# Optimization experiments

Hardware: AMD Instinct MI355X
Metric: run time of the kernel (lower is better)

## Reference

```python
import jax, jax.numpy as jnp
import numpy as np

B, N, IN, HID, RANK, POOL = 128, 512, 512, 512, 64, 8


def setup_inputs() -> dict:
    key = jax.random.key(0)
    ks = jax.random.split(key, 7)
    tree_embedding = jax.random.normal(ks[0], (B, N, IN), dtype=jnp.float32)
    # valid top-down tree: parent(i) < i, parent(0) arbitrary (unused: buffers are zero at t=0)
    rng = np.random.default_rng(0)
    node_connection = jnp.asarray(
        rng.integers(0, np.maximum(np.arange(N), 1), size=(B, N)), dtype=jnp.int32)
    node_mask = jnp.ones((B, N), dtype=bool)
    s = 0.05
    # gate axis g: 0=f, 1=o, 2=z (three DecomposedBilinear modules stacked)
    wl = jax.random.normal(ks[1], (3, POOL, RANK, IN), dtype=jnp.float32) * s
    wr = jax.random.normal(ks[2], (3, POOL, RANK, HID), dtype=jnp.float32) * s
    wo = jax.random.normal(ks[3], (3, HID, POOL), dtype=jnp.float32) * s
    ul = jax.random.normal(ks[4], (3, HID, IN), dtype=jnp.float32) * s   # use_linear on left input
    ur = jax.random.normal(ks[5], (3, HID, HID), dtype=jnp.float32) * s  # use_linear on parent h
    bias = jax.random.normal(ks[6], (3, HID), dtype=jnp.float32) * s    # use_bias
    return dict(tree_embedding=tree_embedding, node_connection=node_connection,
                node_mask=node_mask, wl=wl, wr=wr, wo=wo, ul=ul, ur=ur, bias=bias)


def _gates(emb, ph, wl, wr, wo, ul, ur, bias):
    # Decomposed bilinear for all 3 gates at once.
    # emb: (B, IN), ph: (B, HID)
    lw = jnp.einsum('bi,gpri->gbpr', emb, wl)
    rw = jnp.einsum('bh,gprh->gbpr', ph, wr)
    pooled = jnp.sum(lw * rw, axis=-1)                       # (g, B, POOL)
    out = jnp.einsum('gbp,ghp->gbh', pooled, wo)             # bilinear term
    out = out + jnp.einsum('bi,ghi->gbh', emb, ul)           # linear(left)
    out = out + jnp.einsum('bh,gkh->gbk', ph, ur)            # linear(right); zero when ph==0 (root)
    out = out + bias[:, None, :]
    return out


def _forward(tree_embedding, node_connection, wl, wr, wo, ul, ur, bias):
    batch, node_num, _ = tree_embedding.shape
    hid = wo.shape[1]
    h0 = jnp.zeros((batch, node_num, hid), tree_embedding.dtype)
    c0 = jnp.zeros_like(h0)
    emb_seq = jnp.swapaxes(tree_embedding, 0, 1)   # (N, B, IN)
    par_seq = jnp.swapaxes(node_connection, 0, 1)  # (N, B)

    def step(carry, xs):
        h_buf, c_buf = carry
        t, emb, par = xs
        idx = par[:, None, None].astype(jnp.int32)
        ph = jnp.take_along_axis(h_buf, idx, axis=1)[:, 0]  # parent gather; zeros at t==0
        pc = jnp.take_along_axis(c_buf, idx, axis=1)[:, 0]
        g = _gates(emb, ph, wl, wr, wo, ul, ur, bias)
        f = jax.nn.sigmoid(g[0])
        o = jax.nn.sigmoid(g[1])
        z = jnp.tanh(g[2])
        c = pc * f + (1.0 - f) * z
        h = o * jnp.tanh(c)
        return (h_buf.at[:, t].set(h), c_buf.at[:, t].set(c)), None

    (h_buf, _), _ = jax.lax.scan(step, (h0, c0),
                                 (jnp.arange(node_num), emb_seq, par_seq))
    return h_buf


def reference(tree_embedding, node_connection, node_mask, wl, wr, wo, ul, ur, bias):
    # node_mask is only threaded through the returned state in the torch code; unused here.
    return _forward(tree_embedding, node_connection, wl, wr, wo, ul, ur, bias)
```

## Files before the change

kernel.cpp:

```cpp
#include <hip/hip_runtime.h>

#define NB 128
#define NN 512
#define NODES (NB * NN)
#define NLEVELS 32

typedef __attribute__((ext_vector_type(8))) short short8;
typedef __attribute__((ext_vector_type(4))) short short4v;
typedef __attribute__((ext_vector_type(4))) float f32x4;
typedef unsigned int u32;

__device__ __forceinline__ float bf2f(short s) {
    union { u32 u; float f; } v;
    v.u = ((u32)(unsigned short)s) << 16;
    return v.f;
}
__device__ __forceinline__ short f2bf(float f) {
    union { u32 u; float f; } v;
    v.f = f;
    u32 u = v.u + 0x7FFFu + ((v.u >> 16) & 1u);
    return (short)(u >> 16);
}
__device__ __forceinline__ float fclamp(float x, float lo, float hi) {
    return fminf(fmaxf(x, lo), hi);
}
__device__ __forceinline__ float fsig(float x) {
    return __builtin_amdgcn_rcpf(1.f + __builtin_amdgcn_exp2f(-1.44269504f * x));
}
__device__ __forceinline__ float ftanh(float x) {
    return 1.f - 2.f * __builtin_amdgcn_rcpf(1.f + __builtin_amdgcn_exp2f(2.88539008f * x));
}
#define MFMA16(a, b, c) __builtin_amdgcn_mfma_f32_16x16x32_bf16((a), (b), (c), 0, 0, 0)

__device__ __forceinline__ void gl16(const void* g, void* l) {
    __builtin_amdgcn_global_load_lds(
        (const __attribute__((address_space(1))) unsigned int*)g,
        (__attribute__((address_space(3))) unsigned int*)l,
        16, 0, 0);
}

#define WAIT_VMCNT(n) asm volatile("s_waitcnt vmcnt(" #n ")" ::: "memory")
#define PIPE_BAR()                                  \
    do {                                            \
        __builtin_amdgcn_sched_barrier(0);          \
        __builtin_amdgcn_s_barrier();               \
        __builtin_amdgcn_sched_barrier(0);          \
    } while (0)

__global__ __launch_bounds__(256) void conv_emb_kernel(
    const float* __restrict__ src, const u32* __restrict__ pos_g,
    short* __restrict__ dst)
{
    int i = blockIdx.x * 256 + threadIdx.x;
    const int stride = gridDim.x * 256;
    for (; i < NODES * 64; i += stride) {
        const int node = i >> 6;
        const int o = (i & 63) << 3;
        const u32 dr = pos_g[node];
        const float* s = src + ((size_t)node << 9) + o;
        short8 v;
#pragma unroll
        for (int j = 0; j < 8; j++) v[j] = f2bf(s[j]);
        *(short8*)((char*)dst + ((size_t)dr << 10) + ((size_t)o << 1)) = v;
    }
}

__global__ __launch_bounds__(256) void wpack_lin_kernel(
    const float* __restrict__ ul, const float* __restrict__ ur,
    short* __restrict__ img)
{
    int gid = blockIdx.x * 256 + threadIdx.x;
    const int stride = gridDim.x * 256;
    for (; gid < 196608; gid += stride) {
        const int cgkc = gid / 1536;
        const int d = (gid - cgkc * 1536) << 4;
        const int cg = cgkc >> 4, kc = cgkc & 15;
        const int u = d ^ (((d >> 7) & 7) << 4);
        const int p = u >> 7;
        const int koff = u & 127;
        const int row = ((p >> 6) << 9) + (cg << 6) + (p & 63);
        const float* src = (kc < 8 ? ul : ur) + (size_t)row * 512
                         + ((kc & 7) << 6) + (koff >> 1);
        short8 o;
#pragma unroll
        for (int i = 0; i < 8; i++) o[i] = f2bf(src[i]);
        *(short8*)((char*)img + (size_t)cgkc * 24576 + d) = o;
    }
}
__global__ __launch_bounds__(256) void wpack_pool_kernel(
    const float* __restrict__ wl, const float* __restrict__ wr,
    short* __restrict__ imgL, short* __restrict__ imgR)
{
    int gid = blockIdx.x * 256 + threadIdx.x;
    const int stride = gridDim.x * 256;
    for (; gid < 196608; gid += stride) {
        const int tensor = gid >= 98304;
        const int g2 = gid - tensor * 98304;
        const int sc = g2 / 512;
        const int d = (g2 - sc * 512) << 4;
        const int s = sc >> 3, ch = sc & 7;
        const int slot = d >> 10;
        const int l = (d >> 4) & 63;
        const int col = (slot << 3) + (l >> 3);
        const int eoff = ((l & 7) ^ (col & 7)) << 3;
        const float* src = (tensor ? wr : wl)
                         + (size_t)(s * 64 + col) * 512 + (ch << 6) + eoff;
        short8 o;
#pragma unroll
        for (int i = 0; i < 8; i++) o[i] = f2bf(src[i]);
        short* dst = tensor ? imgR : imgL;
        *(short8*)((char*)dst + (size_t)sc * 8192 + d) = o;
    }
}

__global__ __launch_bounds__(256) void zero_kernel(int* __restrict__ counts)
{
    const int i = blockIdx.x * 256 + threadIdx.x;
    if (i < 520) counts[i] = 0;
}

__global__ __launch_bounds__(256) void depth_kernel(
    const int* __restrict__ conn,
    unsigned char* __restrict__ lvl_g,
    int* __restrict__ counts)
{
    __shared__ short anc[NN];
    __shared__ short dep[NN];
    __shared__ int hist[520];
    const int b = blockIdx.x;
    const int tid = threadIdx.x;

    for (int i = tid; i < 520; i += 256) hist[i] = 0;
    for (int i = tid; i < NN; i += 256) {
        anc[i] = (i == 0) ? (short)0 : (short)conn[b * NN + i];
        dep[i] = (i == 0) ? (short)0 : (short)1;
    }
    __syncthreads();
    for (int it = 0; it < 9; it++) {
        const int i0 = tid, i1 = tid + 256;
        const short a0 = anc[i0], d0 = dep[i0];
        const short a1 = anc[i1], d1 = dep[i1];
        const short da0 = dep[a0], aa0 = anc[a0];
        const short da1 = dep[a1], aa1 = anc[a1];
        __syncthreads();
        dep[i0] = (short)(d0 + da0); anc[i0] = aa0;
        dep[i1] = (short)(d1 + da1); anc[i1] = aa1;
        __syncthreads();
    }
    for (int i = tid; i < NN; i += 256) {
        const unsigned char d = (unsigned char)dep[i];
        lvl_g[b * NN + i] = d;
        atomicAdd(&hist[d], 1);
    }
    __syncthreads();
    for (int i = tid; i < 520; i += 256)
        if (hist[i]) atomicAdd(&counts[i], hist[i]);
}

__global__ __launch_bounds__(256) void scan_kernel(
    const int* __restrict__ counts,
    int* __restrict__ offs,
    int* __restrict__ cursor)
{
    __shared__ int c[520];
    __shared__ int o[520];
    const int tid = threadIdx.x;
    for (int i = tid; i < 520; i += 256) c[i] = counts[i];
    __syncthreads();
    if (tid == 0) {
        int acc = 0;
        for (int l = 0; l < 520; l++) { o[l] = acc; acc += c[l]; }
    }
    __syncthreads();
    for (int i = tid; i < 520; i += 256) {
        offs[i] = o[i];
        cursor[i] = o[i];
    }
}

__global__ __launch_bounds__(256) void scatter_kernel(
    const int* __restrict__ conn,
    const unsigned char* __restrict__ lvl_g,
    int* __restrict__ cursor,
    u32* __restrict__ list,
    u32* __restrict__ pos_g,
    u32* __restrict__ plist)
{
    __shared__ int hist[520];
    __shared__ int base_s[520];
    __shared__ short rank_s[NN];
    __shared__ int pos_s[NN];
    const int b = blockIdx.x;
    const int tid = threadIdx.x;

    for (int i = tid; i < 520; i += 256) hist[i] = 0;
    __syncthreads();
    for (int i = tid; i < NN; i += 256) {
        const int l = lvl_g[b * NN + i];
        rank_s[i] = (short)atomicAdd(&hist[l], 1);
    }
    __syncthreads();
    for (int i = tid; i < 520; i += 256) {
        const int c = hist[i];
        base_s[i] = c ? atomicAdd(&cursor[i], c) : 0;
    }
    __syncthreads();
    for (int i = tid; i < NN; i += 256) {
        const int l = lvl_g[b * NN + i];
        pos_s[i] = base_s[l] + rank_s[i];
    }
    __syncthreads();
    for (int i = tid; i < NN; i += 256) {
        const int par = (i == 0) ? 0 : conn[b * NN + i];
        const int pos = pos_s[i];
        list[pos] = ((u32)b << 18) | ((u32)i << 9) | (u32)par;
        plist[pos] = (u32)pos_s[par];
        pos_g[b * NN + i] = (u32)pos;
    }
}

__global__ __launch_bounds__(256, 2) void pool_kernel(
    const int lvl,
    const short* __restrict__ emb_lvl,
    const short* __restrict__ imgL,
    const short* __restrict__ imgR,
    const short* __restrict__ h_lvl,
    const int* __restrict__ offs,
    const u32* __restrict__ plist,
    float* __restrict__ pooled2)
{
    const int base = offs[lvl];
    const int M = offs[lvl + 1] - base;
    if (M <= 0) return;
    const int nt = (M + 63) >> 6;

    const int s = blockIdx.x % 24;
    const int rb = blockIdx.x / 24;
    const int nb = gridDim.x / 24;
    if (rb >= nt) return;

    __shared__ __attribute__((aligned(16))) char lds[2][32768];

    const int tid = threadIdx.x;
    const int l = tid & 63;
    const int w = tid >> 6;
    const int q = l >> 4;
    const int ln = l & 15;

    const char* bL = (const char*)imgL + (size_t)s * 65536 + (l << 4);
    const char* bR = (const char*)imgR + (size_t)s * 65536 + (l << 4);

    for (int tm = rb; tm < nt; tm += nb) {
        const int m0 = tm << 6;
        const char* pAe[2];
        const char* pAh[2];
#pragma unroll
        for (int cc = 0; cc < 2; cc++) {
            const int row = ((2 * w + cc) << 3) + (l >> 3);
            const int koff = ((l & 7) ^ (row & 7)) << 4;
            int mr = m0 + row; if (mr > M - 1) mr = M - 1;
            pAe[cc] = (const char*)emb_lvl + ((size_t)(base + mr) << 10) + koff;
            pAh[cc] = (const char*)h_lvl + ((size_t)plist[base + mr] << 10) + koff;
        }

        f32x4 accL[4], accR[4];
#pragma unroll
        for (int jj = 0; jj < 4; jj++) {
            accL[jj] = {0.f, 0.f, 0.f, 0.f};
            accR[jj] = {0.f, 0.f, 0.f, 0.f};
        }

        {
            char* L = lds[0];
#pragma unroll
            for (int cc = 0; cc < 2; cc++) {
                const int slt = (2 * w + cc) << 10;
                gl16(pAe[cc], L + slt);
                gl16(pAh[cc], L + 8192 + slt);
                gl16(bL + slt, L + 16384 + slt);
                gl16(bR + slt, L + 24576 + slt);
            }
        }

        for (int c = 0; c < 8; c++) {
            if (c < 7) {
                char* L = lds[(c + 1) & 1];
                const int cb = (c + 1) << 7;
                const size_t ib = (size_t)(c + 1) << 13;
#pragma unroll
                for (int cc = 0; cc < 2; cc++) {
                    const int slt = (2 * w + cc) << 10;
                    gl16(pAe[cc] + cb, L + slt);
                    gl16(pAh[cc] + cb, L + 8192 + slt);
                    gl16(bL + ib + slt, L + 16384 + slt);
                    gl16(bR + ib + slt, L + 24576 + slt);
                }
                WAIT_VMCNT(8);
            } else {
                WAIT_VMCNT(0);
            }
            PIPE_BAR();
            const char* L = lds[c & 1];
#pragma unroll
            for (int kf = 0; kf < 2; kf++) {
                const int abyte = (((w << 4) + ln) << 7) + (kf << 6) + (q << 4);
                const int aswz = abyte ^ ((ln & 7) << 4);
                const short8 ae = *(const short8*)(L + aswz);
                const short8 ah = *(const short8*)(L + 8192 + aswz);
#pragma unroll
                for (int jj = 0; jj < 4; jj++) {
                    const int bbyte = (((jj << 4) + ln) << 7) + (kf << 6) + (q << 4);
                    const int bswz = bbyte ^ ((ln & 7) << 4);
                    const short8 bl = *(const short8*)(L + 16384 + bswz);
                    const short8 br = *(const short8*)(L + 24576 + bswz);
                    accL[jj] = MFMA16(ae, bl, accL[jj]);
                    accR[jj] = MFMA16(ah, br, accR[jj]);
                }
            }
            PIPE_BAR();
        }

#pragma unroll
        for (int reg = 0; reg < 4; reg++) {
            float v = accL[0][reg] * accR[0][reg] + accL[1][reg] * accR[1][reg]
                    + accL[2][reg] * accR[2][reg] + accL[3][reg] * accR[3][reg];
            v += __shfl_xor(v, 1, 64);
            v += __shfl_xor(v, 2, 64);
            v += __shfl_xor(v, 4, 64);
            v += __shfl_xor(v, 8, 64);
            if (ln == 0) {
                const int mr = m0 + (w << 4) + (q << 2) + reg;
                if (mr < M) pooled2[(size_t)mr * 24 + s] = v;
            }
        }
    }
}

__global__ __launch_bounds__(256, 2) void gemm_lin_kernel(
    const int lvl,
    const short* __restrict__ emb_lvl,
    const short* __restrict__ Blin,
    const float* __restrict__ wo,
    const float* __restrict__ bias,
    const int* __restrict__ offs,
    const u32* __restrict__ list,
    const u32* __restrict__ plist,
    const float* __restrict__ pooled2,
    float* __restrict__ h_out,
    short* __restrict__ h_lvl,
    short* __restrict__ c_lvl)
{
    const int base = offs[lvl];
    const int M = offs[lvl + 1] - base;
    if (M <= 0) return;
    const int nt = (M + 127) >> 7;
    const int nkc = (lvl > 0) ? 16 : 8;

    __shared__ __attribute__((aligned(16))) char lds[2][24576];

    const int tid = threadIdx.x;
    const int lane = tid & 63;
    const int w = tid >> 6;
    const int q = lane >> 4;
    const int ln = lane & 15;
    const int x = blockIdx.x & 7;
    const int jb = blockIdx.x >> 3;
    const int cg = jb & 7;
    const int tslot = jb >> 3;
    const int swzc = (ln & 7) << 4;

    const char* pB = (const char*)Blin + (size_t)cg * 393216 + (lane << 4);

    const int wrow0 = w << 5;

    for (int tm = x + (tslot << 3); tm < nt; tm += 96) {
        const int m0 = tm << 7;
        const char *pE0, *pE1, *pH0, *pH1;
        {
            int r0 = m0 + wrow0 + ln;      if (r0 > M - 1) r0 = M - 1;
            int r1 = m0 + wrow0 + 16 + ln; if (r1 > M - 1) r1 = M - 1;
            const int qo = q << 4;
            pE0 = (const char*)emb_lvl + ((size_t)(base + r0) << 10) + qo;
            pE1 = (const char*)emb_lvl + ((size_t)(base + r1) << 10) + qo;
            pH0 = (const char*)h_lvl + ((size_t)plist[base + r0] << 10) + qo;
            pH1 = (const char*)h_lvl + ((size_t)plist[base + r1] << 10) + qo;
        }

        f32x4 acc[2][12];
#pragma unroll
        for (int ms = 0; ms < 2; ms++)
#pragma unroll
            for (int j = 0; j < 12; j++)
                acc[ms][j] = {0.f, 0.f, 0.f, 0.f};

        {
            char* LB = lds[0];
#pragma unroll
            for (int c = 0; c < 6; c++)
                gl16(pB + ((w * 6 + c) << 10), LB + ((w * 6 + c) << 10));
        }
        short8 c00 = *(const short8*)(pE0);
        short8 c01 = *(const short8*)(pE0 + 64);
        short8 c10 = *(const short8*)(pE1);
        short8 c11 = *(const short8*)(pE1 + 64);
        __syncthreads();

        for (int kc = 0; kc < nkc; kc++) {
            const int kn = (kc + 1 < nkc) ? kc + 1 : kc;
            const char* r0 = (kn < 8) ? pE0 : pH0;
            const char* r1 = (kn < 8) ? pE1 : pH1;
            const int cbn = (kn & 7) << 7;
            short8 n00 = *(const short8*)(r0 + cbn);
            short8 n01 = *(const short8*)(r0 + cbn + 64);
            short8 n10 = *(const short8*)(r1 + cbn);
            short8 n11 = *(const short8*)(r1 + cbn + 64);
            if (kc + 1 < nkc) {
                const size_t ib = (size_t)(kc + 1) * 24576;
                char* LB = lds[(kc + 1) & 1];
#pragma unroll
                for (int c = 0; c < 6; c++)
                    gl16(pB + ib + ((w * 6 + c) << 10), LB + ((w * 6 + c) << 10));
            }
            const char* LB = lds[kc & 1];
#pragma unroll
            for (int ks = 0; ks < 2; ks++) {
                const short8 af0 = ks ? c01 : c00;
                const short8 af1 = ks ? c11 : c10;
                const int kb = (ks << 6) + (q << 4);
#pragma unroll
                for (int j = 0; j < 12; j++) {
                    const short8 bf = *(const short8*)(LB + ((((j * 16 + ln) << 7) + kb) ^ swzc));
                    acc[0][j] = MFMA16(af0, bf, acc[0][j]);
                    acc[1][j] = MFMA16(af1, bf, acc[1][j]);
                }
            }
            __syncthreads();
            c00 = n00; c01 = n01; c10 = n10; c11 = n11;
        }

#pragma unroll
        for (int ms = 0; ms < 2; ms++) {
#pragma unroll
            for (int reg = 0; reg < 4; reg++) {
                const int mr = m0 + wrow0 + (ms << 4) + (q << 2) + reg;
                if (mr >= M) continue;
                const u32 pk = list[base + mr];
                const int bb = pk >> 18, tt = (pk >> 9) & 511;
                const u32 ppos = plist[base + mr];
                const float* pr = pooled2 + (size_t)mr * 24;
                const size_t orow = ((size_t)((bb << 9) | tt)) << 9;
                const size_t srow = ((size_t)(base + mr)) << 9;
                const size_t prow = ((size_t)ppos) << 9;
#pragma unroll
                for (int jh = 0; jh < 4; jh++) {
                    const int h = (cg << 6) + (jh << 4) + ln;
                    float v[3];
#pragma unroll
                    for (int g = 0; g < 3; g++) {
                        float xg = acc[ms][(g << 2) + jh][reg] + bias[(g << 9) + h];
                        if (lvl > 0) {
                            const float* wop = wo + ((size_t)((g << 9) + h) << 3);
                            float sdot = 0.f;
#pragma unroll
                            for (int p2 = 0; p2 < 8; p2++)
                                sdot += pr[(g << 3) + p2] * wop[p2];
                            xg += sdot;
                        }
                        v[g] = fclamp(xg, -30.f, 30.f);
                    }
                    const float fg = fsig(v[0]);
                    const float og = fsig(v[1]);
                    const float zg = ftanh(v[2]);
                    float pc = 0.f;
                    if (lvl > 0) {
                        pc = bf2f(c_lvl[prow + h]);
                        pc = fclamp(pc, -1.f, 1.f);
                    }
                    const float cc = pc * fg + (1.f - fg) * zg;
                    const float hh = og * ftanh(cc);
                    c_lvl[srow + h] = f2bf(cc);
                    h_lvl[srow + h] = f2bf(hh);
                    h_out[orow + h] = hh;
                }
            }
        }
    }
}

extern "C" void kernel_launch(void* const* d_in, const int* in_sizes, int n_in,
                              void* d_out, int out_size, void* d_ws, size_t ws_size,
                              hipStream_t stream) {
    const float* emb  = (const float*)d_in[0];
    const int*   conn = (const int*)d_in[1];
    const float* wl   = (const float*)d_in[3];
    const float* wr   = (const float*)d_in[4];
    const float* wo   = (const float*)d_in[5];
    const float* ul   = (const float*)d_in[6];
    const float* ur   = (const float*)d_in[7];
    const float* bias = (const float*)d_in[8];

    char* ws = (char*)d_ws;
    int* offs   = (int*)ws;
    int* counts = offs + 520;
    int* cursor = counts + 520;
    unsigned char* lvl_g = (unsigned char*)(ws + 8192);
    u32* list  = (u32*)(ws + 73728);
    u32* pos_g = (u32*)(ws + 335872);
    u32* plist = (u32*)(ws + 598016);
    short* Blin  = (short*)(ws + 860160);
    short* PimgL = (short*)(ws + 860160 + 3145728);
    short* PimgR = (short*)(ws + 860160 + 4718592);
    short* emb_lvl = (short*)(ws + (8u << 20));
    short* h_lvl = (short*)(ws + (8u << 20) + 67108864u);
    short* c_lvl = (short*)(ws + (8u << 20) + 134217728u);
    float* pooled2 = (float*)(ws + 209715200ull);

    float* h_out = (float*)d_out;

    wpack_lin_kernel<<<dim3(768), dim3(256), 0, stream>>>(ul, ur, Blin);
    wpack_pool_kernel<<<dim3(768), dim3(256), 0, stream>>>(wl, wr, PimgL, PimgR);

    zero_kernel<<<dim3(3), dim3(256), 0, stream>>>(counts);
    depth_kernel<<<dim3(NB), dim3(256), 0, stream>>>(conn, lvl_g, counts);
    scan_kernel<<<dim3(1), dim3(256), 0, stream>>>(counts, offs, cursor);
    scatter_kernel<<<dim3(NB), dim3(256), 0, stream>>>(conn, lvl_g, cursor,
                                                       list, pos_g, plist);
    conv_emb_kernel<<<dim3(2048), dim3(256), 0, stream>>>(emb, pos_g, emb_lvl);

    for (int l = 0; l < NLEVELS; l++) {
        if (l > 0)
            pool_kernel<<<dim3(480), dim3(256), 0, stream>>>(
                l, emb_lvl, PimgL, PimgR, h_lvl, offs, plist, pooled2);
        gemm_lin_kernel<<<dim3(768), dim3(256), 0, stream>>>(
            l, emb_lvl, Blin, wo, bias, offs, list, plist, pooled2,
            h_out, h_lvl, c_lvl);
    }
}
```

Baseline: 1.760 ms.

## Load pool A-operands straight to registers and halve LDS footprint

The pool kernel now loads the emb and parent-h A fragments from global memory directly into registers, prefetching one k-chunk ahead. Only the weight images are staged through LDS, so the LDS buffer shrinks from 64KB to 32KB and the grid doubles to 960 blocks for higher occupancy. The custom vmcnt waits and scheduling barriers are replaced by __syncthreads, which waits on all outstanding loads, including the LDS prefetch just issued. That may reduce load/compute overlap, and the gathered per-lane 16-byte global loads are less coalesced.

```diff
diff --git a/kernel.cpp b/kernel.cpp
--- a/kernel.cpp
+++ b/kernel.cpp
@@ -38,14 +38,6 @@
         (__attribute__((address_space(3))) unsigned int*)l,
         16, 0, 0);
 }
-
-#define WAIT_VMCNT(n) asm volatile("s_waitcnt vmcnt(" #n ")" ::: "memory")
-#define PIPE_BAR()                                  \
-    do {                                            \
-        __builtin_amdgcn_sched_barrier(0);          \
-        __builtin_amdgcn_s_barrier();               \
-        __builtin_amdgcn_sched_barrier(0);          \
-    } while (0)
 
 __global__ __launch_bounds__(256) void conv_emb_kernel(
     const float* __restrict__ src, const u32* __restrict__ pos_g,
@@ -239,7 +231,7 @@
     const int nb = gridDim.x / 24;
     if (rb >= nt) return;
 
-    __shared__ __attribute__((aligned(16))) char lds[2][32768];
+    __shared__ __attribute__((aligned(16))) char lds[2][16384];
 
     const int tid = threadIdx.x;
     const int l = tid & 63;
@@ -252,15 +244,12 @@
 
     for (int tm = rb; tm < nt; tm += nb) {
         const int m0 = tm << 6;
-        const char* pAe[2];
-        const char* pAh[2];
-#pragma unroll
-        for (int cc = 0; cc < 2; cc++) {
-            const int row = ((2 * w + cc) << 3) + (l >> 3);
-            const int koff = ((l & 7) ^ (row & 7)) << 4;
-            int mr = m0 + row; if (mr > M - 1) mr = M - 1;
-            pAe[cc] = (const char*)emb_lvl + ((size_t)(base + mr) << 10) + koff;
-            pAh[cc] = (const char*)h_lvl + ((size_t)plist[base + mr] << 10) + koff;
+        const char *pAe, *pAh;
+        {
+            int r = m0 + (w << 4) + ln; if (r > M - 1) r = M - 1;
+            const int qo = q << 4;
+            pAe = (const char*)emb_lvl + ((size_t)(base + r) << 10) + qo;
+            pAh = (const char*)h_lvl + ((size_t)plist[base + r] << 10) + qo;
         }
 
         f32x4 accL[4], accR[4];
@@ -275,49 +264,50 @@
 #pragma unroll
             for (int cc = 0; cc < 2; cc++) {
                 const int slt = (2 * w + cc) << 10;
-                gl16(pAe[cc], L + slt);
-                gl16(pAh[cc], L + 8192 + slt);
-                gl16(bL + slt, L + 16384 + slt);
-                gl16(bR + slt, L + 24576 + slt);
-            }
-        }
+                gl16(bL + slt, L + slt);
+                gl16(bR + slt, L + 8192 + slt);
+            }
+        }
+        short8 ae0 = *(const short8*)(pAe);
+        short8 ae1 = *(const short8*)(pAe + 64);
+        short8 ah0 = *(const short8*)(pAh);
+        short8 ah1 = *(const short8*)(pAh + 64);
+        __syncthreads();
 
         for (int c = 0; c < 8; c++) {
-            if (c < 7) {
+            const int kn = (c + 1 < 8) ? c + 1 : c;
+            const int cbn = kn << 7;
+            short8 ne0 = *(const short8*)(pAe + cbn);
+            short8 ne1 = *(const short8*)(pAe + cbn + 64);
+            short8 nh0 = *(const short8*)(pAh + cbn);
+            short8 nh1 = *(const short8*)(pAh + cbn + 64);
+            if (c + 1 < 8) {
                 char* L = lds[(c + 1) & 1];
-                const int cb = (c + 1) << 7;
                 const size_t ib = (size_t)(c + 1) << 13;
 #pragma unroll
                 for (int cc = 0; cc < 2; cc++) {
                     const int slt = (2 * w + cc) << 10;
-                    gl16(pAe[cc] + cb, L + slt);
-                    gl16(pAh[cc] + cb, L + 8192 + slt);
-                    gl16(bL + ib + slt, L + 16384 + slt);
-                    gl16(bR + ib + slt, L + 24576 + slt);
+                    gl16(bL + ib + slt, L + slt);
+                    gl16(bR + ib + slt, L + 8192 + slt);
                 }
-                WAIT_VMCNT(8);
-            } else {
-                WAIT_VMCNT(0);
-            }
-            PIPE_BAR();
+            }
             const char* L = lds[c & 1];
 #pragma unroll
             for (int kf = 0; kf < 2; kf++) {
-                const int abyte = (((w << 4) + ln) << 7) + (kf << 6) + (q << 4);
-                const int aswz = abyte ^ ((ln & 7) << 4);
-                const short8 ae = *(const short8*)(L + aswz);
-                const short8 ah = *(const short8*)(L + 8192 + aswz);
+                const short8 ae = kf ? ae1 : ae0;
+                const short8 ah = kf ? ah1 : ah0;
 #pragma unroll
                 for (int jj = 0; jj < 4; jj++) {
                     const int bbyte = (((jj << 4) + ln) << 7) + (kf << 6) + (q << 4);
                     const int bswz = bbyte ^ ((ln & 7) << 4);
-                    const short8 bl = *(const short8*)(L + 16384 + bswz);
-                    const short8 br = *(const short8*)(L + 24576 + bswz);
+                    const short8 bl = *(const short8*)(L + bswz);
+                    const short8 br = *(const short8*)(L + 8192 + bswz);
                     accL[jj] = MFMA16(ae, bl, accL[jj]);
                     accR[jj] = MFMA16(ah, br, accR[jj]);
                 }
             }
-            PIPE_BAR();
+            __syncthreads();
+            ae0 = ne0; ae1 = ne1; ah0 = nh0; ah1 = nh1;
         }
 
 #pragma unroll
@@ -529,7 +519,7 @@
 
     for (int l = 0; l < NLEVELS; l++) {
         if (l > 0)
-            pool_kernel<<<dim3(480), dim3(256), 0, stream>>>(
+            pool_kernel<<<dim3(960), dim3(256), 0, stream>>>(
                 l, emb_lvl, PimgL, PimgR, h_lvl, offs, plist, pooled2);
         gemm_lin_kernel<<<dim3(768), dim3(256), 0, stream>>>(
             l, emb_lvl, Blin, wo, bias, offs, list, plist, pooled2,
```

Measured after the change: 1.953 ms. 11.0% more time.
